# Kernel tuning notes

Hardware: AMD Instinct MI355X
Metric: run time of the kernel (lower is better)

The kernel has to match this reference:

```python
import jax, jax.numpy as jnp
import numpy as np


def setup_inputs() -> dict:
    key = jax.random.key(0)
    k1, k2 = jax.random.split(key)
    pred = jax.random.normal(k1, (4, 8192, 3), dtype=jnp.float32)
    label = jax.random.normal(k2, (4, 8192, 3), dtype=jnp.float32)
    return {"pred": pred, "label": label}


def reference(pred, label):
    # Pairwise Euclidean distances via the Gram-matrix identity
    # explicit repeat+subtract+norm, without the [B,N,M,D] blowup).
    x2 = jnp.sum(pred * pred, axis=-1)            # [B, N]
    y2 = jnp.sum(label * label, axis=-1)          # [B, M]
    xy = jnp.einsum('bnd,bmd->bnm', pred, label)  # [B, N, M]
    d2 = x2[:, :, None] + y2[:, None, :] - 2.0 * xy
    dis = jnp.sqrt(jnp.maximum(d2, 0.0))          # [B, N, M]
    dis_xy = jnp.mean(jnp.min(dis, axis=2))       # pred -> nearest label
    dis_yx = jnp.mean(jnp.min(dis, axis=1))       # label -> nearest pred
    return dis_xy + dis_yx
```

## Files before the change

kernel.cpp:

```cpp
#include <hip/hip_runtime.h>
#include <math.h>

#define BATCH 4
#define NPTS 8192
#define TPB 512
#define RPB 256
#define NBLK (NPTS / RPB)
#define CHUNK_COLS 512
#define NCHUNK (NPTS / CHUNK_COLS)


typedef __attribute__((ext_vector_type(8))) short bf16x8;
typedef __attribute__((ext_vector_type(16))) float f32x16;

static_assert(sizeof(bf16x8) == 16, "frag size");

__device__ inline unsigned short bf16_rne(float v) {
  unsigned u = __builtin_bit_cast(unsigned, v);
  return (unsigned short)((u + 0x7FFFu + ((u >> 16) & 1u)) >> 16);
}
__device__ inline float bf16_up(unsigned short u) {
  return __builtin_bit_cast(float, (unsigned)u << 16);
}

#define ONE_BF16 ((short)0x3F80)
#define HALF_BF16 ((short)0x3F00)
#define QUARTER_BF16 ((short)0x3E80)
#define SIXT_BF16 ((short)0x3D80)

__device__ inline bf16x8 rep8(short s) {
  bf16x8 v;
  v[0] = s; v[1] = s; v[2] = s; v[3] = s;
  v[4] = s; v[5] = s; v[6] = s; v[7] = s;
  return v;
}
__device__ inline bf16x8 pair0(short a, short b) {
  bf16x8 v = {};
  v[0] = a; v[1] = b;
  return v;
}
__device__ inline unsigned pack2(unsigned short lo, unsigned short hi) {
  return (unsigned)lo | ((unsigned)hi << 16);
}

__global__ __launch_bounds__(TPB, 2) void chamfer_main(
    const float* __restrict__ pred, const float* __restrict__ label,
    float* __restrict__ blocksum) {
  __shared__ unsigned lds_w[4][CHUNK_COLS];
  __shared__ unsigned smin_u[RPB];
  __shared__ float ssum[8];

  const int tid = threadIdx.x;
  const int lane = tid & 63;
  const int w = tid >> 6;
  const int rg = w & 3;
  const int ch = w >> 2;
  const int kg = lane >> 5;
  const int b = blockIdx.y;
  const int dir = blockIdx.z;
  const int rowBase = blockIdx.x * RPB;

  const float* __restrict__ rows = dir ? label : pred;
  const float* __restrict__ cols = dir ? pred : label;

  if (tid < RPB) smin_u[tid] = 0x7F800000u;

  bf16x8 aD[2][3];
  bf16x8 a4[2];
#pragma unroll
  for (int rt = 0; rt < 2; ++rt) {
    const int rrow = rowBase + rg * 64 + rt * 32 + (lane & 31);
    const float* p = rows + ((size_t)b * NPTS + rrow) * 3;
    const float x0 = p[0], x1 = p[1], x2 = p[2];
    const unsigned short xh0 = bf16_rne(x0);
    const unsigned short xm0 = bf16_rne(x0 - bf16_up(xh0));
    const unsigned short xh1 = bf16_rne(x1);
    const unsigned short xm1 = bf16_rne(x1 - bf16_up(xh1));
    const unsigned short xh2 = bf16_rne(x2);
    const unsigned short xm2 = bf16_rne(x2 - bf16_up(xh2));
    const float xx = x0 * x0 + x1 * x1 + x2 * x2;
    const unsigned short x2h = bf16_rne(xx);
    const unsigned short x2m = bf16_rne(xx - bf16_up(x2h));
    aD[rt][0] = rep8((short)(kg ? xm0 : xh0));
    aD[rt][1] = rep8((short)(kg ? xm1 : xh1));
    aD[rt][2] = rep8((short)(kg ? xm2 : xh2));
    a4[rt] = kg ? rep8(ONE_BF16) : pair0((short)x2h, (short)x2m);
  }

  const f32x16 zero = {};
  float diag = 0.0f;

  int rowid[16];
  {
    const bf16x8 pa = rep8((short)bf16_rne((float)(lane & 31)));
    const bf16x8 pb = rep8(SIXT_BF16);
    const f32x16 pr = __builtin_amdgcn_mfma_f32_32x32x16_bf16(pa, pb, zero, 0, 0, 0);
#pragma unroll
    for (int i = 0; i < 16; ++i) {
      const float r = pr[i];
      const int ri = (int)(r + 0.5f);
      rowid[i] = ri & 31;
      if (fabsf(r - (float)ri) > 0.01f) diag += 1.0e9f;
    }
  }
  int crossed;
  {
    const bf16x8 pa = rep8(kg ? (short)0 : ONE_BF16);
    const bf16x8 pb = rep8(kg ? HALF_BF16 : QUARTER_BF16);
    const f32x16 ph = __builtin_amdgcn_mfma_f32_32x32x16_bf16(pa, pb, zero, 0, 0, 0);
    const float hp = ph[0];
    crossed = (hp > 3.0f) ? 1 : 0;
    if (fabsf(hp - 2.0f) > 0.05f && fabsf(hp - 4.0f) > 0.05f) diag += 1.0e6f;
  }
  const int bg = kg ^ crossed;

  float mn[2][16];
#pragma unroll
  for (int rt = 0; rt < 2; ++rt)
#pragma unroll
    for (int i = 0; i < 16; ++i) mn[rt][i] = 3.0e38f;

  for (int c = 0; c < NCHUNK; ++c) {
    __syncthreads();
    {
      const float* q = cols + ((size_t)b * NPTS + c * CHUNK_COLS + tid) * 3;
      const float y0 = q[0], y1 = q[1], y2 = q[2];
      const float a0 = -2.0f * y0, a1 = -2.0f * y1, a2 = -2.0f * y2;
      const unsigned short h0 = bf16_rne(a0);
      const unsigned short m0 = bf16_rne(a0 - bf16_up(h0));
      const unsigned short h1 = bf16_rne(a1);
      const unsigned short m1 = bf16_rne(a1 - bf16_up(h1));
      const unsigned short h2 = bf16_rne(a2);
      const unsigned short m2 = bf16_rne(a2 - bf16_up(h2));
      const float qq = y0 * y0 + y1 * y1 + y2 * y2;
      const unsigned short qh = bf16_rne(qq);
      const unsigned short qm = bf16_rne(qq - bf16_up(qh));
      lds_w[0][tid] = pack2(h0, m0);
      lds_w[1][tid] = pack2(h1, m1);
      lds_w[2][tid] = pack2(h2, m2);
      lds_w[3][tid] = pack2(qh, qm);
    }
    __syncthreads();

#pragma unroll
    for (int p = 0; p < 8; p += 2) {
      const int c0 = (ch * 8 + p) * 32 + (lane & 31);
      const int c1 = c0 + 32;
      const unsigned u00 = lds_w[0][c0], u01 = lds_w[1][c0];
      const unsigned u02 = lds_w[2][c0], u0q = lds_w[3][c0];
      const unsigned u10 = lds_w[0][c1], u11 = lds_w[1][c1];
      const unsigned u12 = lds_w[2][c1], u1q = lds_w[3][c1];
      const bf16x8 b00 = pair0((short)(u00 & 0xFFFF), (short)(u00 >> 16));
      const bf16x8 b01 = pair0((short)(u01 & 0xFFFF), (short)(u01 >> 16));
      const bf16x8 b02 = pair0((short)(u02 & 0xFFFF), (short)(u02 >> 16));
      const bf16x8 b0q = bg ? pair0((short)(u0q & 0xFFFF), (short)(u0q >> 16))
                            : rep8(ONE_BF16);
      const bf16x8 b10 = pair0((short)(u10 & 0xFFFF), (short)(u10 >> 16));
      const bf16x8 b11 = pair0((short)(u11 & 0xFFFF), (short)(u11 >> 16));
      const bf16x8 b12 = pair0((short)(u12 & 0xFFFF), (short)(u12 >> 16));
      const bf16x8 b1q = bg ? pair0((short)(u1q & 0xFFFF), (short)(u1q >> 16))
                            : rep8(ONE_BF16);
#pragma unroll
      for (int rt = 0; rt < 2; ++rt) {
        f32x16 A0 = __builtin_amdgcn_mfma_f32_32x32x16_bf16(aD[rt][0], b00, zero, 0, 0, 0);
        A0 = __builtin_amdgcn_mfma_f32_32x32x16_bf16(aD[rt][1], b01, A0, 0, 0, 0);
        A0 = __builtin_amdgcn_mfma_f32_32x32x16_bf16(aD[rt][2], b02, A0, 0, 0, 0);
        A0 = __builtin_amdgcn_mfma_f32_32x32x16_bf16(a4[rt],    b0q, A0, 0, 0, 0);
        f32x16 A1 = __builtin_amdgcn_mfma_f32_32x32x16_bf16(aD[rt][0], b10, zero, 0, 0, 0);
        A1 = __builtin_amdgcn_mfma_f32_32x32x16_bf16(aD[rt][1], b11, A1, 0, 0, 0);
        A1 = __builtin_amdgcn_mfma_f32_32x32x16_bf16(aD[rt][2], b12, A1, 0, 0, 0);
        A1 = __builtin_amdgcn_mfma_f32_32x32x16_bf16(a4[rt],    b1q, A1, 0, 0, 0);
#pragma unroll
        for (int i = 0; i < 16; ++i)
          mn[rt][i] = fminf(fminf(mn[rt][i], A0[i]), A1[i]);
      }
    }
  }

#pragma unroll
  for (int rt = 0; rt < 2; ++rt)
#pragma unroll
    for (int i = 0; i < 16; ++i)
      atomicMin(&smin_u[rg * 64 + rt * 32 + rowid[i]],
                __float_as_uint(mn[rt][i]));
  __syncthreads();

  float v = diag;
  if (tid < RPB) v += sqrtf(fmaxf(__uint_as_float(smin_u[tid]), 0.0f));
#pragma unroll
  for (int off = 32; off > 0; off >>= 1) v += __shfl_down(v, off, 64);
  if (lane == 0) ssum[w] = v;
  __syncthreads();
  if (tid == 0) {
    blocksum[((size_t)dir * BATCH + b) * NBLK + blockIdx.x] =
        ssum[0] + ssum[1] + ssum[2] + ssum[3] +
        ssum[4] + ssum[5] + ssum[6] + ssum[7];
  }
}

__global__ __launch_bounds__(256) void chamfer_finish(
    const float* __restrict__ blocksum, float* __restrict__ out) {
  float v = blocksum[threadIdx.x];
#pragma unroll
  for (int off = 32; off > 0; off >>= 1) v += __shfl_down(v, off, 64);
  __shared__ float s4[4];
  const int wid = threadIdx.x >> 6;
  const int lane = threadIdx.x & 63;
  if (lane == 0) s4[wid] = v;
  __syncthreads();
  if (threadIdx.x == 0)
    out[0] = (s4[0] + s4[1] + s4[2] + s4[3]) * (1.0f / (float)(BATCH * NPTS));
}

extern "C" void kernel_launch(void* const* d_in, const int* in_sizes, int n_in,
                              void* d_out, int out_size, void* d_ws,
                              size_t ws_size, hipStream_t stream) {
  const float* pred = (const float*)d_in[0];
  const float* label = (const float*)d_in[1];
  float* out = (float*)d_out;
  float* blocksum = (float*)d_ws;

  chamfer_main<<<dim3(NBLK, BATCH, 2), TPB, 0, stream>>>(pred, label, blocksum);
  chamfer_finish<<<1, 256, 0, stream>>>(blocksum, out);
}
```

Before: 112.4 us.

## Pack split-bf16 distance terms into two K=16 MFMAs per tile

Restructures the MFMA formulation so the hi/lo split-bf16 products and squared-norm terms are packed along the K dimension, using two MFMAs per 32x32 tile instead of four. It probes the K-lane mapping at runtime to place operands correctly. Columns are staged in LDS as 16-byte vectors and the running minimum uses v_min3. Rows per block drop to 128 so each wave owns one row tile, with launch bounds raised for occupancy, so the block count doubles and the finish kernel reduces 512 partials. The packed formulation drops some cross terms (e.g. lo*lo) and relies on the probed K layout being correct.

```diff
diff --git a/kernel.cpp b/kernel.cpp
--- a/kernel.cpp
+++ b/kernel.cpp
@@ -4,7 +4,7 @@
 #define BATCH 4
 #define NPTS 8192
 #define TPB 512
-#define RPB 256
+#define RPB 128
 #define NBLK (NPTS / RPB)
 #define CHUNK_COLS 512
 #define NCHUNK (NPTS / CHUNK_COLS)
@@ -24,8 +24,6 @@
 }
 
 #define ONE_BF16 ((short)0x3F80)
-#define HALF_BF16 ((short)0x3F00)
-#define QUARTER_BF16 ((short)0x3E80)
 #define SIXT_BF16 ((short)0x3D80)
 
 __device__ inline bf16x8 rep8(short s) {
@@ -34,19 +32,11 @@
   v[4] = s; v[5] = s; v[6] = s; v[7] = s;
   return v;
 }
-__device__ inline bf16x8 pair0(short a, short b) {
-  bf16x8 v = {};
-  v[0] = a; v[1] = b;
-  return v;
-}
-__device__ inline unsigned pack2(unsigned short lo, unsigned short hi) {
-  return (unsigned)lo | ((unsigned)hi << 16);
-}
-
-__global__ __launch_bounds__(TPB, 2) void chamfer_main(
+
+__global__ __launch_bounds__(TPB, 4) void chamfer_main(
     const float* __restrict__ pred, const float* __restrict__ label,
     float* __restrict__ blocksum) {
-  __shared__ unsigned lds_w[4][CHUNK_COLS];
+  __shared__ __align__(1024) char stage[16 * 1024];
   __shared__ unsigned smin_u[RPB];
   __shared__ float ssum[8];
 
@@ -65,11 +55,51 @@
 
   if (tid < RPB) smin_u[tid] = 0x7F800000u;
 
-  bf16x8 aD[2][3];
-  bf16x8 a4[2];
-#pragma unroll
-  for (int rt = 0; rt < 2; ++rt) {
-    const int rrow = rowBase + rg * 64 + rt * 32 + (lane & 31);
+  const f32x16 zero = {};
+  float diag = 0.0f;
+
+  int beta[16];
+  {
+    bf16x8 pa;
+#pragma unroll
+    for (int e = 0; e < 8; ++e)
+      pa[e] = (short)((unsigned short)((127 + e + 8 * kg) << 7));
+    unsigned hit = 0;
+#pragma unroll
+    for (int h = 0; h < 2; ++h)
+#pragma unroll
+      for (int m = 0; m < 8; ++m) {
+        bf16x8 pb = rep8(0);
+        if (kg == h) pb[m] = ONE_BF16;
+        const f32x16 pr =
+            __builtin_amdgcn_mfma_f32_32x32x16_bf16(pa, pb, zero, 0, 0, 0);
+        const unsigned bits = __float_as_uint(pr[0]);
+        const int s = (int)((bits >> 23) & 0xFFu) - 127;
+        beta[h * 8 + m] = s & 15;
+        hit |= 1u << (s & 15);
+        if ((bits & 0x7FFFFFu) != 0u || s < 0 || s > 15) diag += 1.0e9f;
+      }
+    if (hit != 0xFFFFu) diag += 1.0e9f;
+  }
+
+  int rowid[16];
+  {
+    const bf16x8 pa = rep8((short)bf16_rne((float)(lane & 31)));
+    const bf16x8 pb = rep8(SIXT_BF16);
+    const f32x16 pr =
+        __builtin_amdgcn_mfma_f32_32x32x16_bf16(pa, pb, zero, 0, 0, 0);
+#pragma unroll
+    for (int i = 0; i < 16; ++i) {
+      const float r = pr[i];
+      const int ri = (int)(r + 0.5f);
+      rowid[i] = ri & 31;
+      if (fabsf(r - (float)ri) > 0.01f) diag += 1.0e9f;
+    }
+  }
+
+  bf16x8 aHI, aLO;
+  {
+    const int rrow = rowBase + rg * 32 + (lane & 31);
     const float* p = rows + ((size_t)b * NPTS + rrow) * 3;
     const float x0 = p[0], x1 = p[1], x2 = p[2];
     const unsigned short xh0 = bf16_rne(x0);
@@ -81,44 +111,29 @@
     const float xx = x0 * x0 + x1 * x1 + x2 * x2;
     const unsigned short x2h = bf16_rne(xx);
     const unsigned short x2m = bf16_rne(xx - bf16_up(x2h));
-    aD[rt][0] = rep8((short)(kg ? xm0 : xh0));
-    aD[rt][1] = rep8((short)(kg ? xm1 : xh1));
-    aD[rt][2] = rep8((short)(kg ? xm2 : xh2));
-    a4[rt] = kg ? rep8(ONE_BF16) : pair0((short)x2h, (short)x2m);
-  }
-
-  const f32x16 zero = {};
-  float diag = 0.0f;
-
-  int rowid[16];
-  {
-    const bf16x8 pa = rep8((short)bf16_rne((float)(lane & 31)));
-    const bf16x8 pb = rep8(SIXT_BF16);
-    const f32x16 pr = __builtin_amdgcn_mfma_f32_32x32x16_bf16(pa, pb, zero, 0, 0, 0);
-#pragma unroll
-    for (int i = 0; i < 16; ++i) {
-      const float r = pr[i];
-      const int ri = (int)(r + 0.5f);
-      rowid[i] = ri & 31;
-      if (fabsf(r - (float)ri) > 0.01f) diag += 1.0e9f;
-    }
-  }
-  int crossed;
-  {
-    const bf16x8 pa = rep8(kg ? (short)0 : ONE_BF16);
-    const bf16x8 pb = rep8(kg ? HALF_BF16 : QUARTER_BF16);
-    const f32x16 ph = __builtin_amdgcn_mfma_f32_32x32x16_bf16(pa, pb, zero, 0, 0, 0);
-    const float hp = ph[0];
-    crossed = (hp > 3.0f) ? 1 : 0;
-    if (fabsf(hp - 2.0f) > 0.05f && fabsf(hp - 4.0f) > 0.05f) diag += 1.0e6f;
-  }
-  const int bg = kg ^ crossed;
-
-  float mn[2][16];
-#pragma unroll
-  for (int rt = 0; rt < 2; ++rt)
-#pragma unroll
-    for (int i = 0; i < 16; ++i) mn[rt][i] = 3.0e38f;
+    const unsigned short LAHI[8] = {xh0, xh1, xh2, x2h,
+                                    (unsigned short)0x3F80, 0, 0, 0};
+    const unsigned short LALO[8] = {xh0, xm0, xh1, xm1, xh2, xm2, x2m,
+                                    (unsigned short)0x3F80};
+    unsigned short avH[8] = {0, 0, 0, 0, 0, 0, 0, 0};
+    unsigned short avL[8] = {0, 0, 0, 0, 0, 0, 0, 0};
+#pragma unroll
+    for (int m = 0; m < 8; ++m) {
+      const int s = beta[m];
+      if ((s >> 3) == kg) {
+        avH[s & 7] = LAHI[m];
+        avL[s & 7] = LALO[m];
+      }
+    }
+#pragma unroll
+    for (int e = 0; e < 8; ++e) { aHI[e] = (short)avH[e]; aLO[e] = (short)avL[e]; }
+  }
+
+  float mn[16];
+#pragma unroll
+  for (int i = 0; i < 16; ++i) mn[i] = 3.0e38f;
+
+  const bf16x8 bzero = rep8(0);
 
   for (int c = 0; c < NCHUNK; ++c) {
     __syncthreads();
@@ -135,54 +150,37 @@
       const float qq = y0 * y0 + y1 * y1 + y2 * y2;
       const unsigned short qh = bf16_rne(qq);
       const unsigned short qm = bf16_rne(qq - bf16_up(qh));
-      lds_w[0][tid] = pack2(h0, m0);
-      lds_w[1][tid] = pack2(h1, m1);
-      lds_w[2][tid] = pack2(h2, m2);
-      lds_w[3][tid] = pack2(qh, qm);
+      bf16x8 gH, gL;
+      gH[0] = (short)h0; gH[1] = (short)h1; gH[2] = (short)h2; gH[3] = ONE_BF16;
+      gH[4] = (short)qh; gH[5] = 0;         gH[6] = 0;         gH[7] = 0;
+      gL[0] = (short)m0; gL[1] = (short)h0; gL[2] = (short)m1; gL[3] = (short)h1;
+      gL[4] = (short)m2; gL[5] = (short)h2; gL[6] = ONE_BF16;  gL[7] = (short)qm;
+      char* bp = &stage[(tid >> 5) * 1024 + (tid & 31) * 16];
+      *(bf16x8*)bp = gH;
+      *(bf16x8*)(bp + 512) = gL;
     }
     __syncthreads();
 
 #pragma unroll
     for (int p = 0; p < 8; p += 2) {
-      const int c0 = (ch * 8 + p) * 32 + (lane & 31);
-      const int c1 = c0 + 32;
-      const unsigned u00 = lds_w[0][c0], u01 = lds_w[1][c0];
-      const unsigned u02 = lds_w[2][c0], u0q = lds_w[3][c0];
-      const unsigned u10 = lds_w[0][c1], u11 = lds_w[1][c1];
-      const unsigned u12 = lds_w[2][c1], u1q = lds_w[3][c1];
-      const bf16x8 b00 = pair0((short)(u00 & 0xFFFF), (short)(u00 >> 16));
-      const bf16x8 b01 = pair0((short)(u01 & 0xFFFF), (short)(u01 >> 16));
-      const bf16x8 b02 = pair0((short)(u02 & 0xFFFF), (short)(u02 >> 16));
-      const bf16x8 b0q = bg ? pair0((short)(u0q & 0xFFFF), (short)(u0q >> 16))
-                            : rep8(ONE_BF16);
-      const bf16x8 b10 = pair0((short)(u10 & 0xFFFF), (short)(u10 >> 16));
-      const bf16x8 b11 = pair0((short)(u11 & 0xFFFF), (short)(u11 >> 16));
-      const bf16x8 b12 = pair0((short)(u12 & 0xFFFF), (short)(u12 >> 16));
-      const bf16x8 b1q = bg ? pair0((short)(u1q & 0xFFFF), (short)(u1q >> 16))
-                            : rep8(ONE_BF16);
-#pragma unroll
-      for (int rt = 0; rt < 2; ++rt) {
-        f32x16 A0 = __builtin_amdgcn_mfma_f32_32x32x16_bf16(aD[rt][0], b00, zero, 0, 0, 0);
-        A0 = __builtin_amdgcn_mfma_f32_32x32x16_bf16(aD[rt][1], b01, A0, 0, 0, 0);
-        A0 = __builtin_amdgcn_mfma_f32_32x32x16_bf16(aD[rt][2], b02, A0, 0, 0, 0);
-        A0 = __builtin_amdgcn_mfma_f32_32x32x16_bf16(a4[rt],    b0q, A0, 0, 0, 0);
-        f32x16 A1 = __builtin_amdgcn_mfma_f32_32x32x16_bf16(aD[rt][0], b10, zero, 0, 0, 0);
-        A1 = __builtin_amdgcn_mfma_f32_32x32x16_bf16(aD[rt][1], b11, A1, 0, 0, 0);
-        A1 = __builtin_amdgcn_mfma_f32_32x32x16_bf16(aD[rt][2], b12, A1, 0, 0, 0);
-        A1 = __builtin_amdgcn_mfma_f32_32x32x16_bf16(a4[rt],    b1q, A1, 0, 0, 0);
-#pragma unroll
-        for (int i = 0; i < 16; ++i)
-          mn[rt][i] = fminf(fminf(mn[rt][i], A0[i]), A1[i]);
-      }
-    }
-  }
-
-#pragma unroll
-  for (int rt = 0; rt < 2; ++rt)
-#pragma unroll
-    for (int i = 0; i < 16; ++i)
-      atomicMin(&smin_u[rg * 64 + rt * 32 + rowid[i]],
-                __float_as_uint(mn[rt][i]));
+      const char* rd0 = &stage[(ch * 8 + p) * 1024 + (lane & 31) * 16];
+      const bf16x8 bH0 = kg ? bzero : *(const bf16x8*)rd0;
+      const bf16x8 bL0 = kg ? bzero : *(const bf16x8*)(rd0 + 512);
+      const bf16x8 bH1 = kg ? bzero : *(const bf16x8*)(rd0 + 1024);
+      const bf16x8 bL1 = kg ? bzero : *(const bf16x8*)(rd0 + 1536);
+      f32x16 t0 = __builtin_amdgcn_mfma_f32_32x32x16_bf16(aHI, bH0, zero, 0, 0, 0);
+      t0 = __builtin_amdgcn_mfma_f32_32x32x16_bf16(aLO, bL0, t0, 0, 0, 0);
+      f32x16 t1 = __builtin_amdgcn_mfma_f32_32x32x16_bf16(aHI, bH1, zero, 0, 0, 0);
+      t1 = __builtin_amdgcn_mfma_f32_32x32x16_bf16(aLO, bL1, t1, 0, 0, 0);
+#pragma unroll
+      for (int i = 0; i < 16; ++i)
+        asm("v_min3_f32 %0, %0, %1, %2" : "+v"(mn[i]) : "v"(t0[i]), "v"(t1[i]));
+    }
+  }
+
+#pragma unroll
+  for (int i = 0; i < 16; ++i)
+    atomicMin(&smin_u[rg * 32 + rowid[i]], __float_as_uint(mn[i]));
   __syncthreads();
 
   float v = diag;
@@ -198,18 +196,19 @@
   }
 }
 
-__global__ __launch_bounds__(256) void chamfer_finish(
+__global__ __launch_bounds__(512) void chamfer_finish(
     const float* __restrict__ blocksum, float* __restrict__ out) {
   float v = blocksum[threadIdx.x];
 #pragma unroll
   for (int off = 32; off > 0; off >>= 1) v += __shfl_down(v, off, 64);
-  __shared__ float s4[4];
+  __shared__ float s8[8];
   const int wid = threadIdx.x >> 6;
   const int lane = threadIdx.x & 63;
-  if (lane == 0) s4[wid] = v;
+  if (lane == 0) s8[wid] = v;
   __syncthreads();
   if (threadIdx.x == 0)
-    out[0] = (s4[0] + s4[1] + s4[2] + s4[3]) * (1.0f / (float)(BATCH * NPTS));
+    out[0] = (s8[0] + s8[1] + s8[2] + s8[3] + s8[4] + s8[5] + s8[6] + s8[7]) *
+             (1.0f / (float)(BATCH * NPTS));
 }
 
 extern "C" void kernel_launch(void* const* d_in, const int* in_sizes, int n_in,
@@ -221,5 +220,5 @@
   float* blocksum = (float*)d_ws;
 
   chamfer_main<<<dim3(NBLK, BATCH, 2), TPB, 0, stream>>>(pred, label, blocksum);
-  chamfer_finish<<<1, 256, 0, stream>>>(blocksum, out);
-}
+  chamfer_finish<<<1, 512, 0, stream>>>(blocksum, out);
+}
```

After: 146.0 us. +29.8%, slower.
